# Kernel tuning notes

Hardware: AMD Instinct MI355X
Metric: run time of the kernel (lower is better)

## Reference

```python
import jax, jax.numpy as jnp
import numpy as np

N_REGS, R_BIT, N_OPS, FLIP = 8, 16, 16, 2

def bit2dec(bits):
    # little-endian soft bits -> decimal: sum_k b_k * 2^k
    k = jnp.arange(bits.shape[-1], dtype=bits.dtype)
    return jnp.sum(bits * jnp.exp2(k), axis=-1)

def addr_w(idx, n):
    # differentiable soft one-hot over n slots (linear interpolation kernel)
    grid = jnp.arange(n, dtype=idx.dtype)
    return jnp.maximum(1.0 - jnp.abs(idx[..., None] - grid), 0.0)

def setup_inputs():
    key = jax.random.key(0)
    ks = jax.random.split(key, 12)
    B, H, I, L = 8192, 512, 1024, 16
    return dict(
        z_hidden=jax.random.normal(ks[0], (B, H), jnp.float32),
        P_op=jax.random.uniform(ks[1], (B, L, 4), dtype=jnp.float32),
        P_dst=jax.random.uniform(ks[2], (B, L, 3), dtype=jnp.float32),
        P_src1=jax.random.uniform(ks[3], (B, L, 3), dtype=jnp.float32),
        P_src2=jax.random.uniform(ks[4], (B, L, 3), dtype=jnp.float32),
        P_imm=jax.random.uniform(ks[5], (B, L, 3), dtype=jnp.float32),
        Proglen=jax.random.uniform(ks[6], (B, 4), dtype=jnp.float32),
        group_num=16,
        W1=jax.random.normal(ks[7], (H, I), jnp.float32) / np.sqrt(H).astype(np.float32),
        b1=jnp.zeros((I,), jnp.float32),
        WR=jax.random.normal(ks[8], (I, N_REGS * R_BIT), jnp.float32) / np.sqrt(I).astype(np.float32),
        bR=jnp.zeros((N_REGS * R_BIT,), jnp.float32),
        Wt=jax.random.normal(ks[9], (I, 1), jnp.float32) / np.sqrt(I).astype(np.float32),
        bt=jnp.zeros((1,), jnp.float32),
        W_r2h=jax.random.normal(ks[10], (N_REGS, H), jnp.float32) / np.sqrt(N_REGS).astype(np.float32),
        b_r2h=jnp.zeros((H,), jnp.float32),
        ln_g=jnp.ones((H,), jnp.float32),
        ln_b=jnp.zeros((H,), jnp.float32),
    )

def reference(z_hidden, P_op, P_dst, P_src1, P_src2, P_imm, Proglen, group_num,
              W1, b1, WR, bR, Wt, bt, W_r2h, b_r2h, ln_g, ln_b):
    B, L, G = z_hidden.shape[0], P_op.shape[1], group_num
    # ---- Augmentation_Layer: MLP head -> R soft-bits + threshold ----
    h = jax.nn.relu(z_hidden @ W1 + b1)
    R_bits = jax.nn.sigmoid(h @ WR + bR).reshape(B, N_REGS, R_BIT)
    threshold = jax.nn.sigmoid(h @ Wt + bt)                 # [B,1]
    # ---- GroupSample.generate4R: flip FLIP random R-bits per candidate (cand 0 = original) ----
    idx = jax.random.randint(jax.random.key(42), (B, G, FLIP), 0, N_REGS * R_BIT)
    mask = jnp.clip(jax.nn.one_hot(idx, N_REGS * R_BIT, dtype=jnp.float32).sum(-2), 0.0, 1.0)
    mask = mask.at[:, 0].set(0.0).reshape(B, G, N_REGS, R_BIT)
    Rb = R_bits[:, None]                                    # [B,1,n_regs,r_bit]
    R = bit2dec(Rb + mask * (1.0 - 2.0 * Rb))               # [B,G,n_regs] decimals
    M = jnp.zeros_like(R)
    prog_len = jnp.broadcast_to(bit2dec(Proglen)[:, None], (B, G))
    dec = lambda x: bit2dec(x).T                            # [L,B]
    prog = (dec(P_op), dec(P_dst), dec(P_src1), dec(P_src2), dec(P_imm),
            jnp.arange(L, dtype=jnp.float32))

    # ---- MultiInterpreter: differentiable soft register machine ----
    def step(carry, xs):
        R, M = carry
        op_t, dst_t, s1_t, s2_t, imm_t, t = xs
        bc = lambda v: jnp.broadcast_to(v[:, None], (B, G))
        op_t, dst_t, s1_t, s2_t, imm_t = map(bc, (op_t, dst_t, s1_t, s2_t, imm_t))
        active = jnp.clip(prog_len - t, 0.0, 1.0)           # halt mask [B,G]
        w_d = addr_w(dst_t, N_REGS)                         # [B,G,n_regs]
        w_1 = addr_w(s1_t, N_REGS)
        w_2 = addr_w(s2_t, N_REGS)
        w_op = addr_w(op_t, N_OPS)                          # [B,G,16]
        r1 = jnp.sum(w_1 * R, -1); r2 = jnp.sum(w_2 * R, -1)
        m1 = jnp.sum(w_1 * M, -1); old = jnp.sum(w_d * R, -1)
        results = jnp.stack([
            old,                       # 0 NOP
            r1 + r2,                   # 1 ADD
            r1 - r2,                   # 2 SUB
            r1 * r2 / 65536.0,         # 3 MUL (scaled by 2^r_bit)
            r1,                        # 4 MOV
            imm_t,                     # 5 LOADI
            r1 + imm_t,                # 6 ADDI
            jnp.maximum(r1, r2),       # 7 MAX
            jnp.minimum(r1, r2),       # 8 MIN
            -r1,                       # 9 NEG
            0.5 * r1,                  # 10 SHR
            r2,                        # 11 MOV2
            m1,                        # 12 LOAD M[src1]
            old,                       # 13 STORE (reg unchanged)
            jnp.abs(r1),               # 14 ABS
            old,                       # 15 NOP
        ], axis=-1)
        res = jnp.sum(w_op * results, -1)                   # [B,G]
        p_store = w_op[..., 13]
        R = R + active[..., None] * w_d * (res[..., None] - R)
        M = M + (active * p_store)[..., None] * w_d * (r1[..., None] - M)
        return (R, M), None

    (R, M), _ = jax.lax.scan(step, (R, M), prog)
    # ---- register2hidden + LayerNorm ----
    reg_hidden = R @ W_r2h + b_r2h                          # [B,G,H]
    mu = reg_hidden.mean(-1, keepdims=True)
    var = reg_hidden.var(-1, keepdims=True)
    reg_hidden = (reg_hidden - mu) * jax.lax.rsqrt(var + 1e-5) * ln_g + ln_b
    return reg_hidden, threshold
```

## Files before the change

### kernel.cpp

```cpp
#include <hip/hip_runtime.h>
#include <stdint.h>

typedef __attribute__((ext_vector_type(8))) short short8;
typedef __attribute__((ext_vector_type(4))) float f32x4;
typedef __attribute__((ext_vector_type(8))) unsigned short ushort8;
typedef __attribute__((ext_vector_type(4))) unsigned short ushort4v;

__device__ __forceinline__ unsigned short f2bf(float f) {
  uint32_t u = __float_as_uint(f);
  uint32_t r = (u + 0x7fffu + ((u >> 16) & 1u)) >> 16;
  return (unsigned short)r;
}
__device__ __forceinline__ float bf2f(unsigned short v) {
  return __uint_as_float(((uint32_t)v) << 16);
}

typedef __attribute__((address_space(1))) const unsigned int g_u32;
typedef __attribute__((address_space(3))) unsigned int l_u32;
__device__ __forceinline__ void gl_lds16(const void* g, void* l) {
  __builtin_amdgcn_global_load_lds((g_u32*)g, (l_u32*)l, 16, 0, 0);
}

__device__ __forceinline__ uint32_t rotl32(uint32_t v, int d) { return (v << d) | (v >> (32 - d)); }

__device__ __forceinline__ void threefry2x32(uint32_t k0, uint32_t k1, uint32_t& x0, uint32_t& x1) {
  const uint32_t ks2 = k0 ^ k1 ^ 0x1BD11BDAu;
  x0 += k0; x1 += k1;
  x0 += x1; x1 = rotl32(x1, 13); x1 ^= x0;
  x0 += x1; x1 = rotl32(x1, 15); x1 ^= x0;
  x0 += x1; x1 = rotl32(x1, 26); x1 ^= x0;
  x0 += x1; x1 = rotl32(x1, 6);  x1 ^= x0;
  x0 += k1; x1 += ks2 + 1u;
  x0 += x1; x1 = rotl32(x1, 17); x1 ^= x0;
  x0 += x1; x1 = rotl32(x1, 29); x1 ^= x0;
  x0 += x1; x1 = rotl32(x1, 16); x1 ^= x0;
  x0 += x1; x1 = rotl32(x1, 24); x1 ^= x0;
  x0 += ks2; x1 += k0 + 2u;
  x0 += x1; x1 = rotl32(x1, 13); x1 ^= x0;
  x0 += x1; x1 = rotl32(x1, 15); x1 ^= x0;
  x0 += x1; x1 = rotl32(x1, 26); x1 ^= x0;
  x0 += x1; x1 = rotl32(x1, 6);  x1 ^= x0;
  x0 += k0; x1 += k1 + 3u;
  x0 += x1; x1 = rotl32(x1, 17); x1 ^= x0;
  x0 += x1; x1 = rotl32(x1, 29); x1 ^= x0;
  x0 += x1; x1 = rotl32(x1, 16); x1 ^= x0;
  x0 += x1; x1 = rotl32(x1, 24); x1 ^= x0;
  x0 += k1; x1 += ks2 + 4u;
  x0 += x1; x1 = rotl32(x1, 13); x1 ^= x0;
  x0 += x1; x1 = rotl32(x1, 15); x1 ^= x0;
  x0 += x1; x1 = rotl32(x1, 26); x1 ^= x0;
  x0 += x1; x1 = rotl32(x1, 6);  x1 ^= x0;
  x0 += ks2; x1 += k0 + 5u;
}

__global__ __launch_bounds__(256) void prep_kernel(const float* __restrict__ z,
                                                   unsigned short* __restrict__ zb, int n8,
                                                   const float* __restrict__ W1,
                                                   const float* __restrict__ WR,
                                                   unsigned short* __restrict__ W1t,
                                                   unsigned short* __restrict__ WRt,
                                                   const float* __restrict__ P_op,
                                                   const float* __restrict__ P_dst,
                                                   const float* __restrict__ P_s1,
                                                   const float* __restrict__ P_s2,
                                                   const float* __restrict__ P_imm,
                                                   const float* __restrict__ Plen,
                                                   float* __restrict__ prog,
                                                   float* __restrict__ plen, int BT) {
  __shared__ float t[32][33];
  const int tid = threadIdx.x;
  const int bx = blockIdx.x;
  if (bx < 2048) {
    const int i = bx * 256 + tid;
    if (i >= n8) return;
    const float4 a = reinterpret_cast<const float4*>(z)[i * 2];
    const float4 b = reinterpret_cast<const float4*>(z)[i * 2 + 1];
    ushort8 u;
    u[0] = f2bf(a.x); u[1] = f2bf(a.y); u[2] = f2bf(a.z); u[3] = f2bf(a.w);
    u[4] = f2bf(b.x); u[5] = f2bf(b.y); u[6] = f2bf(b.z); u[7] = f2bf(b.w);
    reinterpret_cast<ushort8*>(zb)[i] = u;
  } else if (bx < 2688) {
    const int b = bx - 2048;
    const float* src; unsigned short* dst; int N, K, k0, n0;
    if (b < 512) {
      src = W1; dst = W1t; N = 1024; K = 512;
      k0 = (b & 15) * 32; n0 = (b >> 4) * 32;
    } else {
      const int b2 = b - 512;
      src = WR; dst = WRt; N = 128; K = 1024;
      k0 = (b2 & 31) * 32; n0 = (b2 >> 5) * 32;
    }
    {
      const int row = tid >> 3, c4 = (tid & 7) * 4;
      const float4 v = *reinterpret_cast<const float4*>(&src[(size_t)(k0 + row) * N + n0 + c4]);
      t[row][c4] = v.x; t[row][c4 + 1] = v.y; t[row][c4 + 2] = v.z; t[row][c4 + 3] = v.w;
    }
    __syncthreads();
    {
      const int n = tid >> 3, k4 = (tid & 7) * 4;
      ushort4v o;
      o.x = f2bf(t[k4 + 0][n]); o.y = f2bf(t[k4 + 1][n]);
      o.z = f2bf(t[k4 + 2][n]); o.w = f2bf(t[k4 + 3][n]);
      *reinterpret_cast<ushort4v*>(&dst[(size_t)(n0 + n) * K + k0 + k4]) = o;
    }
  } else {
    const int i = (bx - 2688) * 256 + tid;
    if (i >= BT) return;
    const float* po = P_op + (size_t)i * 4;
    const float op = po[0] + 2.f * po[1] + 4.f * po[2] + 8.f * po[3];
    const float* pd = P_dst + (size_t)i * 3;
    const float dv = pd[0] + 2.f * pd[1] + 4.f * pd[2];
    const float* p1 = P_s1 + (size_t)i * 3;
    const float s1v = p1[0] + 2.f * p1[1] + 4.f * p1[2];
    const float* p2 = P_s2 + (size_t)i * 3;
    const float s2v = p2[0] + 2.f * p2[1] + 4.f * p2[2];
    const float* pi = P_imm + (size_t)i * 3;
    const float imv = pi[0] + 2.f * pi[1] + 4.f * pi[2];
    float* o = prog + (size_t)i * 5;
    o[0] = op; o[1] = dv; o[2] = s1v; o[3] = s2v; o[4] = imv;
    if ((i & 15) == 0) {
      const int b = i >> 4;
      const float* pl = Plen + (size_t)b * 4;
      plen[b] = pl[0] + 2.f * pl[1] + 4.f * pl[2] + 8.f * pl[3];
    }
  }
}

__global__ __launch_bounds__(256) void gemm_fused(const unsigned short* __restrict__ zb,
                                                  const unsigned short* __restrict__ W1t,
                                                  const float* __restrict__ b1,
                                                  const unsigned short* __restrict__ WRt,
                                                  const float* __restrict__ Wt,
                                                  float* __restrict__ part,
                                                  float* __restrict__ thr_part, int B) {
  __shared__ __align__(16) char smem[34816];
  unsigned short* AsF = (unsigned short*)smem;
  unsigned short* BsF = (unsigned short*)(smem + 16384);
  auto H2 = reinterpret_cast<unsigned short (*)[136]>(smem);

  const int tid = threadIdx.x;
  const int lane = tid & 63, wave = tid >> 6;
  const int wm = wave >> 1, wn = wave & 1;
  const int wgid = blockIdx.x;
  const int work = (wgid & 7) * 64 + (wgid >> 3);
  const int by = work >> 3, bx = work & 7;
  const int bm = by * 128, bn = bx * 128;

  f32x4 acc[4][4];
#pragma unroll
  for (int i = 0; i < 4; ++i)
#pragma unroll
    for (int j = 0; j < 4; ++j) acc[i][j] = (f32x4)0.f;

  const int fr = lane & 15, kc = (lane >> 4) * 8;
  const int lr = (lane >> 4) * 4, lc = lane & 15;
  const int lrow = lane >> 3, slot = lane & 7;
  const int sslot = (slot ^ lrow) << 3;
  const int fx = fr & 7;
  const int cbase = lane >> 4;

  for (int k0 = 0; k0 < 512; k0 += 64) {
#pragma unroll
    for (int i = 0; i < 4; ++i) {
      const int r0 = wave * 32 + i * 8;
      gl_lds16(&zb[(size_t)(bm + r0 + lrow) * 512 + k0 + sslot], &AsF[r0 * 64]);
    }
#pragma unroll
    for (int i = 0; i < 4; ++i) {
      const int r0 = wave * 32 + i * 8;
      gl_lds16(&W1t[(size_t)(bn + r0 + lrow) * 512 + k0 + sslot], &BsF[r0 * 64]);
    }
    __syncthreads();
#pragma unroll
    for (int s = 0; s < 2; ++s) {
      short8 af[4], bfv[4];
#pragma unroll
      for (int f = 0; f < 4; ++f) {
        const int row = wm * 64 + f * 16 + fr;
        const int c = s * 4 + cbase;
        af[f] = *reinterpret_cast<const short8*>(&AsF[row * 64 + ((c ^ fx) << 3)]);
      }
#pragma unroll
      for (int f = 0; f < 4; ++f) {
        const int row = wn * 64 + f * 16 + fr;
        const int c = s * 4 + cbase;
        bfv[f] = *reinterpret_cast<const short8*>(&BsF[row * 64 + ((c ^ fx) << 3)]);
      }
#pragma unroll
      for (int fm = 0; fm < 4; ++fm)
#pragma unroll
        for (int fn = 0; fn < 4; ++fn)
          acc[fm][fn] = __builtin_amdgcn_mfma_f32_16x16x32_bf16(af[fm], bfv[fn], acc[fm][fn], 0, 0, 0);
    }
    __syncthreads();
  }

#pragma unroll
  for (int fn = 0; fn < 4; ++fn) {
    const int col_l = wn * 64 + fn * 16 + lc;
    const float bv = b1[bn + col_l];
#pragma unroll
    for (int fm = 0; fm < 4; ++fm) {
      const int row_l0 = wm * 64 + fm * 16 + lr;
#pragma unroll
      for (int r = 0; r < 4; ++r)
        H2[row_l0 + r][col_l] = f2bf(fmaxf(acc[fm][fn][r] + bv, 0.f));
    }
  }
  __syncthreads();

  {
    const int row = tid >> 1, half = tid & 1;
    const unsigned short* hp = &H2[row][half * 64];
    const float* wp = &Wt[bn + half * 64];
    float s = 0.f;
#pragma unroll
    for (int j = 0; j < 8; ++j) {
      const ushort8 a = *reinterpret_cast<const ushort8*>(hp + j * 8);
      const float4 w0 = *reinterpret_cast<const float4*>(wp + j * 8);
      const float4 w1 = *reinterpret_cast<const float4*>(wp + j * 8 + 4);
      s += bf2f(a[0]) * w0.x + bf2f(a[1]) * w0.y + bf2f(a[2]) * w0.z + bf2f(a[3]) * w0.w;
      s += bf2f(a[4]) * w1.x + bf2f(a[5]) * w1.y + bf2f(a[6]) * w1.z + bf2f(a[7]) * w1.w;
    }
    s += __shfl_xor(s, 1);
    if (half == 0) thr_part[(size_t)bx * B + bm + row] = s;
  }

  f32x4 acc2[4][4];
#pragma unroll
  for (int i = 0; i < 4; ++i)
#pragma unroll
    for (int j = 0; j < 4; ++j) acc2[i][j] = (f32x4)0.f;

#pragma unroll
  for (int ks = 0; ks < 4; ++ks) {
    short8 af2[4], bf2v[4];
#pragma unroll
    for (int fm = 0; fm < 4; ++fm)
      af2[fm] = *reinterpret_cast<const short8*>(&H2[wm * 64 + fm * 16 + fr][ks * 32 + kc]);
#pragma unroll
    for (int fn = 0; fn < 4; ++fn)
      bf2v[fn] = *reinterpret_cast<const short8*>(
          &WRt[(size_t)(wn * 64 + fn * 16 + fr) * 1024 + bn + ks * 32 + kc]);
#pragma unroll
    for (int fm = 0; fm < 4; ++fm)
#pragma unroll
      for (int fn = 0; fn < 4; ++fn)
        acc2[fm][fn] = __builtin_amdgcn_mfma_f32_16x16x32_bf16(af2[fm], bf2v[fn], acc2[fm][fn], 0, 0, 0);
  }

  float* pp = part + (size_t)bx * B * 128;
#pragma unroll
  for (int fn = 0; fn < 4; ++fn) {
    const int col = wn * 64 + fn * 16 + lc;
#pragma unroll
    for (int fm = 0; fm < 4; ++fm) {
      const int row0 = bm + wm * 64 + fm * 16 + lr;
#pragma unroll
      for (int r = 0; r < 4; ++r)
        pp[(size_t)(row0 + r) * 128 + col] = acc2[fm][fn][r];
    }
  }
}

__global__ __launch_bounds__(256) void scan2_kernel(const float* __restrict__ part,
                                                    const float* __restrict__ bR,
                                                    const float* __restrict__ thr_part,
                                                    const float* __restrict__ bt,
                                                    const float* __restrict__ prog,
                                                    const float* __restrict__ plen,
                                                    float* __restrict__ Rfinal,
                                                    float* __restrict__ thr_out, int B) {
  __shared__ float s_bits[16][128];
  __shared__ float s_prog[16][80];
  __shared__ float s_plen[16];
  const int tid = threadIdx.x;
  const int b0 = blockIdx.x * 16;
#pragma unroll
  for (int j = 0; j < 8; ++j) {
    const int f = tid + 256 * j;
    const int lb = f >> 7, c = f & 127;
    float s = part[(size_t)(b0 + lb) * 128 + c];
#pragma unroll
    for (int sl = 1; sl < 8; ++sl)
      s += part[(size_t)sl * B * 128 + (size_t)(b0 + lb) * 128 + c];
    s_bits[lb][c] = 1.f / (1.f + expf(-(s + bR[c])));
  }
#pragma unroll
  for (int j = 0; j < 5; ++j) {
    const int f = tid + 256 * j;
    s_prog[f / 80][f % 80] = prog[(size_t)b0 * 80 + f];
  }
  if (tid < 16) {
    s_plen[tid] = plen[b0 + tid];
    float s = thr_part[b0 + tid];
#pragma unroll
    for (int sl = 1; sl < 8; ++sl) s += thr_part[(size_t)sl * B + b0 + tid];
    thr_out[b0 + tid] = 1.f / (1.f + expf(-(s + bt[0])));
  }
  __syncthreads();

  const int lb = tid >> 4, g = tid & 15;
  const int bg = (b0 + lb) * 16 + g;

  uint32_t k2a, k2b;
  { uint32_t x0 = 0u, x1 = 1u; threefry2x32(0u, 42u, x0, x1); k2a = x0; k2b = x1; }
  uint32_t p0, p1;
  {
    uint32_t x0 = 0u, x1 = (uint32_t)bg * 2u;
    threefry2x32(k2a, k2b, x0, x1);
    p0 = (x0 ^ x1) & 127u;
  }
  {
    uint32_t x0 = 0u, x1 = (uint32_t)bg * 2u + 1u;
    threefry2x32(k2a, k2b, x0, x1);
    p1 = (x0 ^ x1) & 127u;
  }

  float R[8], M[8];
#pragma unroll
  for (int r = 0; r < 8; ++r) {
    float a = 0.f;
#pragma unroll
    for (int bit = 0; bit < 16; ++bit) {
      const int pos = r * 16 + bit;
      float v = s_bits[lb][pos];
      const bool flip = (g != 0) && ((int)p0 == pos || (int)p1 == pos);
      v = flip ? 1.0f - v : v;
      a = fmaf(v, (float)(1 << bit), a);
    }
    R[r] = a;
    M[r] = 0.f;
  }

  const float pl = s_plen[lb];
  for (int t = 0; t < 16; ++t) {
    const float op = s_prog[lb][t * 5 + 0];
    const float dst = s_prog[lb][t * 5 + 1];
    const float sa = s_prog[lb][t * 5 + 2];
    const float sb = s_prog[lb][t * 5 + 3];
    const float imm = s_prog[lb][t * 5 + 4];
    const float active = fminf(fmaxf(pl - (float)t, 0.f), 1.f);
    float r1 = 0.f, r2 = 0.f, m1 = 0.f, old = 0.f;
    float wd[8];
#pragma unroll
    for (int i = 0; i < 8; ++i) {
      const float w1 = fmaxf(1.f - fabsf(sa - (float)i), 0.f);
      const float w2 = fmaxf(1.f - fabsf(sb - (float)i), 0.f);
      wd[i] = fmaxf(1.f - fabsf(dst - (float)i), 0.f);
      r1 = fmaf(w1, R[i], r1);
      r2 = fmaf(w2, R[i], r2);
      m1 = fmaf(w1, M[i], m1);
      old = fmaf(wd[i], R[i], old);
    }
    float results[16];
    results[0] = old;               results[1] = r1 + r2;
    results[2] = r1 - r2;           results[3] = r1 * r2 * (1.f / 65536.f);
    results[4] = r1;                results[5] = imm;
    results[6] = r1 + imm;          results[7] = fmaxf(r1, r2);
    results[8] = fminf(r1, r2);     results[9] = -r1;
    results[10] = 0.5f * r1;        results[11] = r2;
    results[12] = m1;               results[13] = old;
    results[14] = fabsf(r1);        results[15] = old;
    float res = 0.f;
    const float pstore = fmaxf(1.f - fabsf(op - 13.f), 0.f);
#pragma unroll
    for (int o = 0; o < 16; ++o) res = fmaf(fmaxf(1.f - fabsf(op - (float)o), 0.f), results[o], res);
#pragma unroll
    for (int i = 0; i < 8; ++i) {
      R[i] = fmaf(active * wd[i], res - R[i], R[i]);
      M[i] = fmaf(active * pstore * wd[i], r1 - M[i], M[i]);
    }
  }

  float* outp = Rfinal + (size_t)bg * 8;
  *reinterpret_cast<float4*>(outp) = make_float4(R[0], R[1], R[2], R[3]);
  *reinterpret_cast<float4*>(outp + 4) = make_float4(R[4], R[5], R[6], R[7]);
}

__global__ __launch_bounds__(256) void final_expand2(const float* __restrict__ Rf,
                                                     const float* __restrict__ W,
                                                     const float* __restrict__ bias,
                                                     const float* __restrict__ gam,
                                                     const float* __restrict__ bet,
                                                     float* __restrict__ out, int rowsPerWave) {
  const int lane = threadIdx.x & 63;
  const int w = blockIdx.x * 4 + (threadIdx.x >> 6);
  const int cA = lane * 4, cB = 256 + lane * 4;

  float wreg[8][8];
#pragma unroll
  for (int reg = 0; reg < 8; ++reg) {
    const float4 wa = *reinterpret_cast<const float4*>(&W[reg * 512 + cA]);
    const float4 wb = *reinterpret_cast<const float4*>(&W[reg * 512 + cB]);
    wreg[reg][0] = wa.x; wreg[reg][1] = wa.y; wreg[reg][2] = wa.z; wreg[reg][3] = wa.w;
    wreg[reg][4] = wb.x; wreg[reg][5] = wb.y; wreg[reg][6] = wb.z; wreg[reg][7] = wb.w;
  }
  float bi[8], ga[8], be[8];
  {
    const float4 a = *reinterpret_cast<const float4*>(&bias[cA]);
    const float4 b = *reinterpret_cast<const float4*>(&bias[cB]);
    bi[0] = a.x; bi[1] = a.y; bi[2] = a.z; bi[3] = a.w; bi[4] = b.x; bi[5] = b.y; bi[6] = b.z; bi[7] = b.w;
    const float4 c = *reinterpret_cast<const float4*>(&gam[cA]);
    const float4 d = *reinterpret_cast<const float4*>(&gam[cB]);
    ga[0] = c.x; ga[1] = c.y; ga[2] = c.z; ga[3] = c.w; ga[4] = d.x; ga[5] = d.y; ga[6] = d.z; ga[7] = d.w;
    const float4 e = *reinterpret_cast<const float4*>(&bet[cA]);
    const float4 f = *reinterpret_cast<const float4*>(&bet[cB]);
    be[0] = e.x; be[1] = e.y; be[2] = e.z; be[3] = e.w; be[4] = f.x; be[5] = f.y; be[6] = f.z; be[7] = f.w;
  }

  const int r0 = w * rowsPerWave;
#pragma unroll 2
  for (int i = 0; i < 8; ++i) {
    const int row = r0 + i;
    const float4 ra = *reinterpret_cast<const float4*>(&Rf[(size_t)row * 8]);
    const float4 rb = *reinterpret_cast<const float4*>(&Rf[(size_t)row * 8 + 4]);
    const float r[8] = {ra.x, ra.y, ra.z, ra.w, rb.x, rb.y, rb.z, rb.w};
    float x[8];
#pragma unroll
    for (int j = 0; j < 8; ++j) x[j] = bi[j];
#pragma unroll
    for (int reg = 0; reg < 8; ++reg)
#pragma unroll
      for (int j = 0; j < 8; ++j) x[j] = fmaf(r[reg], wreg[reg][j], x[j]);
    float s1 = 0.f, s2 = 0.f;
#pragma unroll
    for (int j = 0; j < 8; ++j) { s1 += x[j]; s2 = fmaf(x[j], x[j], s2); }
#pragma unroll
    for (int off = 32; off; off >>= 1) { s1 += __shfl_xor(s1, off); s2 += __shfl_xor(s2, off); }
    const float mean = s1 * (1.f / 512.f);
    const float var = s2 * (1.f / 512.f) - mean * mean;
    const float inv = rsqrtf(var + 1e-5f);
    float y[8];
#pragma unroll
    for (int j = 0; j < 8; ++j) y[j] = (x[j] - mean) * inv * ga[j] + be[j];
    float* dst = out + (size_t)row * 512;
    *reinterpret_cast<float4*>(dst + cA) = make_float4(y[0], y[1], y[2], y[3]);
    *reinterpret_cast<float4*>(dst + cB) = make_float4(y[4], y[5], y[6], y[7]);
  }
}

extern "C" void kernel_launch(void* const* d_in, const int* in_sizes, int n_in,
                              void* d_out, int out_size, void* d_ws, size_t ws_size,
                              hipStream_t stream) {
  const float* z    = (const float*)d_in[0];
  const float* P_op = (const float*)d_in[1];
  const float* P_dst= (const float*)d_in[2];
  const float* P_s1 = (const float*)d_in[3];
  const float* P_s2 = (const float*)d_in[4];
  const float* P_imm= (const float*)d_in[5];
  const float* Plen = (const float*)d_in[6];
  const float* W1   = (const float*)d_in[8];
  const float* b1   = (const float*)d_in[9];
  const float* WR   = (const float*)d_in[10];
  const float* bR   = (const float*)d_in[11];
  const float* Wt   = (const float*)d_in[12];
  const float* bt   = (const float*)d_in[13];
  const float* W_r2h= (const float*)d_in[14];
  const float* b_r2h= (const float*)d_in[15];
  const float* ln_g = (const float*)d_in[16];
  const float* ln_b = (const float*)d_in[17];

  const int B = in_sizes[0] / 512;
  float* out = (float*)d_out;
  float* part    = out + (size_t)(1 << 25);
  float* thr_out = out + (size_t)B * 16 * 512;

  float* ws = (float*)d_ws;
  float* prog   = ws;
  float* plen   = prog + (size_t)B * 80;
  float* Rfinal = plen + B;
  float* thr_part = Rfinal + (size_t)B * 128;
  unsigned short* W1t = (unsigned short*)(thr_part + (size_t)8 * B);
  unsigned short* WRt = W1t + (size_t)1024 * 512;
  unsigned short* zb  = WRt + (size_t)128 * 1024;

  const dim3 blk(256);
  prep_kernel<<<dim3(3200), blk, 0, stream>>>(z, zb, B * 512 / 8, W1, WR, W1t, WRt,
                                              P_op, P_dst, P_s1, P_s2, P_imm, Plen,
                                              prog, plen, B * 16);
  gemm_fused<<<dim3(512), blk, 0, stream>>>(zb, W1t, b1, WRt, Wt, part, thr_part, B);
  scan2_kernel<<<dim3(B / 16), blk, 0, stream>>>(part, bR, thr_part, bt, prog, plen, Rfinal,
                                                 thr_out, B);
  final_expand2<<<dim3(B * 16 / 4 / 8), blk, 0, stream>>>(Rfinal, W_r2h, b_r2h, ln_g, ln_b, out,
                                                          8);
}
```

Measured before the change: 109.3 us.

## Fuse register scan with register-to-hidden projection and LayerNorm

Adds a scan_expand kernel that runs the soft-register program scan for 4 batch rows (64 candidates) per block, keeps the final registers in shared memory, and directly performs the 8x512 projection plus LayerNorm before writing the output. This removes the Rfinal round-trip and one kernel launch. The GEMM partial sums move from the tail of the output buffer into workspace, with the old two-kernel path kept as a fallback when the workspace is too small. Only 64 of 256 threads do the serial scan, so occupancy during that phase is low.

```diff
diff --git a/kernel.cpp b/kernel.cpp
--- a/kernel.cpp
+++ b/kernel.cpp
@@ -263,6 +263,183 @@
   }
 }
 
+__global__ __launch_bounds__(256) void scan_expand(const float* __restrict__ part,
+                                                   const float* __restrict__ bR,
+                                                   const float* __restrict__ thr_part,
+                                                   const float* __restrict__ bt,
+                                                   const float* __restrict__ prog,
+                                                   const float* __restrict__ plen,
+                                                   const float* __restrict__ W,
+                                                   const float* __restrict__ bias,
+                                                   const float* __restrict__ gam,
+                                                   const float* __restrict__ bet,
+                                                   float* __restrict__ thr_out,
+                                                   float* __restrict__ out, int B) {
+  __shared__ float s_bits[4][128];
+  __shared__ float s_prog[4][80];
+  __shared__ float s_plen[4];
+  __shared__ float Rs[64][8];
+  const int tid = threadIdx.x;
+  const int lane = tid & 63, wave = tid >> 6;
+  const int b0 = blockIdx.x * 4;
+
+  {
+#pragma unroll
+    for (int e = 0; e < 2; ++e) {
+      const int ff = tid * 2 + e;
+      const int lb = ff >> 7, c = ff & 127;
+      float s = part[(size_t)(b0 + lb) * 128 + c];
+#pragma unroll
+      for (int sl = 1; sl < 8; ++sl)
+        s += part[(size_t)sl * B * 128 + (size_t)(b0 + lb) * 128 + c];
+      s_bits[lb][c] = 1.f / (1.f + expf(-(s + bR[c])));
+    }
+  }
+#pragma unroll
+  for (int j = 0; j < 2; ++j) {
+    const int f = tid + 256 * j;
+    if (f < 320) s_prog[f / 80][f % 80] = prog[(size_t)b0 * 80 + f];
+  }
+  if (tid < 4) {
+    s_plen[tid] = plen[b0 + tid];
+    float s = thr_part[b0 + tid];
+#pragma unroll
+    for (int sl = 1; sl < 8; ++sl) s += thr_part[(size_t)sl * B + b0 + tid];
+    thr_out[b0 + tid] = 1.f / (1.f + expf(-(s + bt[0])));
+  }
+  __syncthreads();
+
+  if (tid < 64) {
+    const int lb = tid >> 4, g = tid & 15;
+    const int bg = (b0 + lb) * 16 + g;
+
+    uint32_t k2a, k2b;
+    { uint32_t x0 = 0u, x1 = 1u; threefry2x32(0u, 42u, x0, x1); k2a = x0; k2b = x1; }
+    uint32_t p0, p1;
+    {
+      uint32_t x0 = 0u, x1 = (uint32_t)bg * 2u;
+      threefry2x32(k2a, k2b, x0, x1);
+      p0 = (x0 ^ x1) & 127u;
+    }
+    {
+      uint32_t x0 = 0u, x1 = (uint32_t)bg * 2u + 1u;
+      threefry2x32(k2a, k2b, x0, x1);
+      p1 = (x0 ^ x1) & 127u;
+    }
+
+    float R[8], M[8];
+#pragma unroll
+    for (int r = 0; r < 8; ++r) {
+      float a = 0.f;
+#pragma unroll
+      for (int bit = 0; bit < 16; ++bit) {
+        const int pos = r * 16 + bit;
+        float v = s_bits[lb][pos];
+        const bool flip = (g != 0) && ((int)p0 == pos || (int)p1 == pos);
+        v = flip ? 1.0f - v : v;
+        a = fmaf(v, (float)(1 << bit), a);
+      }
+      R[r] = a;
+      M[r] = 0.f;
+    }
+
+    const float pl = s_plen[lb];
+    for (int t = 0; t < 16; ++t) {
+      const float op = s_prog[lb][t * 5 + 0];
+      const float dst = s_prog[lb][t * 5 + 1];
+      const float sa = s_prog[lb][t * 5 + 2];
+      const float sbv = s_prog[lb][t * 5 + 3];
+      const float imm = s_prog[lb][t * 5 + 4];
+      const float active = fminf(fmaxf(pl - (float)t, 0.f), 1.f);
+      float r1 = 0.f, r2 = 0.f, m1 = 0.f, old = 0.f;
+      float wd[8];
+#pragma unroll
+      for (int i = 0; i < 8; ++i) {
+        const float w1 = fmaxf(1.f - fabsf(sa - (float)i), 0.f);
+        const float w2 = fmaxf(1.f - fabsf(sbv - (float)i), 0.f);
+        wd[i] = fmaxf(1.f - fabsf(dst - (float)i), 0.f);
+        r1 = fmaf(w1, R[i], r1);
+        r2 = fmaf(w2, R[i], r2);
+        m1 = fmaf(w1, M[i], m1);
+        old = fmaf(wd[i], R[i], old);
+      }
+      float results[16];
+      results[0] = old;               results[1] = r1 + r2;
+      results[2] = r1 - r2;           results[3] = r1 * r2 * (1.f / 65536.f);
+      results[4] = r1;                results[5] = imm;
+      results[6] = r1 + imm;          results[7] = fmaxf(r1, r2);
+      results[8] = fminf(r1, r2);     results[9] = -r1;
+      results[10] = 0.5f * r1;        results[11] = r2;
+      results[12] = m1;               results[13] = old;
+      results[14] = fabsf(r1);        results[15] = old;
+      float res = 0.f;
+      const float pstore = fmaxf(1.f - fabsf(op - 13.f), 0.f);
+#pragma unroll
+      for (int o = 0; o < 16; ++o) res = fmaf(fmaxf(1.f - fabsf(op - (float)o), 0.f), results[o], res);
+#pragma unroll
+      for (int i = 0; i < 8; ++i) {
+        R[i] = fmaf(active * wd[i], res - R[i], R[i]);
+        M[i] = fmaf(active * pstore * wd[i], r1 - M[i], M[i]);
+      }
+    }
+#pragma unroll
+    for (int r = 0; r < 8; ++r) Rs[tid][r] = R[r];
+  }
+  __syncthreads();
+
+  const int cA = lane * 4, cB = 256 + lane * 4;
+  float wreg[8][8];
+#pragma unroll
+  for (int reg = 0; reg < 8; ++reg) {
+    const float4 wa = *reinterpret_cast<const float4*>(&W[reg * 512 + cA]);
+    const float4 wb = *reinterpret_cast<const float4*>(&W[reg * 512 + cB]);
+    wreg[reg][0] = wa.x; wreg[reg][1] = wa.y; wreg[reg][2] = wa.z; wreg[reg][3] = wa.w;
+    wreg[reg][4] = wb.x; wreg[reg][5] = wb.y; wreg[reg][6] = wb.z; wreg[reg][7] = wb.w;
+  }
+  float bi[8], ga[8], be[8];
+  {
+    const float4 a = *reinterpret_cast<const float4*>(&bias[cA]);
+    const float4 b = *reinterpret_cast<const float4*>(&bias[cB]);
+    bi[0] = a.x; bi[1] = a.y; bi[2] = a.z; bi[3] = a.w; bi[4] = b.x; bi[5] = b.y; bi[6] = b.z; bi[7] = b.w;
+    const float4 c = *reinterpret_cast<const float4*>(&gam[cA]);
+    const float4 d = *reinterpret_cast<const float4*>(&gam[cB]);
+    ga[0] = c.x; ga[1] = c.y; ga[2] = c.z; ga[3] = c.w; ga[4] = d.x; ga[5] = d.y; ga[6] = d.z; ga[7] = d.w;
+    const float4 e = *reinterpret_cast<const float4*>(&bet[cA]);
+    const float4 f = *reinterpret_cast<const float4*>(&bet[cB]);
+    be[0] = e.x; be[1] = e.y; be[2] = e.z; be[3] = e.w; be[4] = f.x; be[5] = f.y; be[6] = f.z; be[7] = f.w;
+  }
+
+  const size_t rowbase = (size_t)blockIdx.x * 64;
+#pragma unroll 2
+  for (int i = 0; i < 16; ++i) {
+    const int rl = wave * 16 + i;
+    float r[8];
+#pragma unroll
+    for (int j = 0; j < 8; ++j) r[j] = Rs[rl][j];
+    float x[8];
+#pragma unroll
+    for (int j = 0; j < 8; ++j) x[j] = bi[j];
+#pragma unroll
+    for (int reg = 0; reg < 8; ++reg)
+#pragma unroll
+      for (int j = 0; j < 8; ++j) x[j] = fmaf(r[reg], wreg[reg][j], x[j]);
+    float s1 = 0.f, s2 = 0.f;
+#pragma unroll
+    for (int j = 0; j < 8; ++j) { s1 += x[j]; s2 = fmaf(x[j], x[j], s2); }
+#pragma unroll
+    for (int off = 32; off; off >>= 1) { s1 += __shfl_xor(s1, off); s2 += __shfl_xor(s2, off); }
+    const float mean = s1 * (1.f / 512.f);
+    const float var = s2 * (1.f / 512.f) - mean * mean;
+    const float inv = rsqrtf(var + 1e-5f);
+    float y[8];
+#pragma unroll
+    for (int j = 0; j < 8; ++j) y[j] = (x[j] - mean) * inv * ga[j] + be[j];
+    float* dst = out + (rowbase + rl) * 512;
+    *reinterpret_cast<float4*>(dst + cA) = make_float4(y[0], y[1], y[2], y[3]);
+    *reinterpret_cast<float4*>(dst + cB) = make_float4(y[4], y[5], y[6], y[7]);
+  }
+}
+
 __global__ __launch_bounds__(256) void scan2_kernel(const float* __restrict__ part,
                                                     const float* __restrict__ bR,
                                                     const float* __restrict__ thr_part,
@@ -463,7 +640,6 @@
 
   const int B = in_sizes[0] / 512;
   float* out = (float*)d_out;
-  float* part    = out + (size_t)(1 << 25);
   float* thr_out = out + (size_t)B * 16 * 512;
 
   float* ws = (float*)d_ws;
@@ -474,14 +650,24 @@
   unsigned short* W1t = (unsigned short*)(thr_part + (size_t)8 * B);
   unsigned short* WRt = W1t + (size_t)1024 * 512;
   unsigned short* zb  = WRt + (size_t)128 * 1024;
+  float* part_ws = (float*)(zb + (size_t)B * 512);
+
+  const size_t need = (size_t)((char*)(part_ws + (size_t)8 * B * 128) - (char*)d_ws);
+  const bool fuse = ws_size >= need;
+  float* part = fuse ? part_ws : (out + (size_t)(1 << 25));
 
   const dim3 blk(256);
   prep_kernel<<<dim3(3200), blk, 0, stream>>>(z, zb, B * 512 / 8, W1, WR, W1t, WRt,
                                               P_op, P_dst, P_s1, P_s2, P_imm, Plen,
                                               prog, plen, B * 16);
   gemm_fused<<<dim3(512), blk, 0, stream>>>(zb, W1t, b1, WRt, Wt, part, thr_part, B);
-  scan2_kernel<<<dim3(B / 16), blk, 0, stream>>>(part, bR, thr_part, bt, prog, plen, Rfinal,
-                                                 thr_out, B);
-  final_expand2<<<dim3(B * 16 / 4 / 8), blk, 0, stream>>>(Rfinal, W_r2h, b_r2h, ln_g, ln_b, out,
-                                                          8);
-}
+  if (fuse) {
+    scan_expand<<<dim3(B / 4), blk, 0, stream>>>(part, bR, thr_part, bt, prog, plen,
+                                                 W_r2h, b_r2h, ln_g, ln_b, thr_out, out, B);
+  } else {
+    scan2_kernel<<<dim3(B / 16), blk, 0, stream>>>(part, bR, thr_part, bt, prog, plen, Rfinal,
+                                                   thr_out, B);
+    final_expand2<<<dim3(B * 16 / 4 / 8), blk, 0, stream>>>(Rfinal, W_r2h, b_r2h, ln_g, ln_b, out,
+                                                            8);
+  }
+}
```

Measured after the change: 111.7 us. +2.2%, slower.
